# Kernel tuning notes

Measured on AMD Instinct MI355X. Metric: run time of the kernel, lower is better.

The kernel has to match this reference:

```python
import jax, jax.numpy as jnp
import numpy as np

N = 100000   # nodes
E = 1600000  # edges (before self-loops)
H1, C1 = 8, 16   # conv1: heads=8, out_channels=16
H2, C2 = 1, 1    # conv2: heads=1, out_channels=1
NEG_SLOPE = 0.2
EPS = 1e-16


def setup_inputs() -> dict:
    key = jax.random.key(0)
    ks = jax.random.split(key, 10)
    s = 0.3
    return {
        "x": jax.random.normal(ks[0], (N, 1), jnp.float32),
        "edge_index": jax.random.randint(ks[1], (2, E), 0, N, dtype=jnp.int64),
        "W1": jax.random.normal(ks[2], (1, H1 * C1), jnp.float32) * s,
        "att_src1": jax.random.normal(ks[3], (1, H1, C1), jnp.float32) * s,
        "att_dst1": jax.random.normal(ks[4], (1, H1, C1), jnp.float32) * s,
        "b1": jax.random.normal(ks[5], (H1 * C1,), jnp.float32) * s,
        "W2": jax.random.normal(ks[6], (H1 * C1, H2 * C2), jnp.float32) * s,
        "att_src2": jax.random.normal(ks[7], (1, H2, C2), jnp.float32) * s,
        "att_dst2": jax.random.normal(ks[8], (1, H2, C2), jnp.float32) * s,
        "b2": jax.random.normal(ks[9], (C2,), jnp.float32) * s,
    }


def gat_conv(x, src, dst, W, att_src, att_dst, bias, heads, ch, concat):
    # Linear projection, split into heads: [N, H, C]
    h = (x @ W).reshape(-1, heads, ch)
    # Per-node attention logits: [N, H]
    a_src = (h * att_src).sum(-1)
    a_dst = (h * att_dst).sum(-1)
    # Edge-wise score with LeakyReLU: [E, H]
    e = jax.nn.leaky_relu(a_src[src] + a_dst[dst], NEG_SLOPE)
    # Segment softmax over incoming edges of each dst node
    m = jax.ops.segment_max(e, dst, num_segments=N)
    ex = jnp.exp(e - m[dst])
    denom = jax.ops.segment_sum(ex, dst, num_segments=N)
    alpha = ex / (denom[dst] + EPS)                      # [E, H]
    # Weighted scatter-add aggregation: [N, H, C]
    out = jax.ops.segment_sum(h[src] * alpha[:, :, None], dst, num_segments=N)
    out = out.reshape(-1, heads * ch) if concat else out.mean(axis=1)
    return out + bias


def reference(x, edge_index, W1, att_src1, att_dst1, b1, W2, att_src2, att_dst2, b2):
    # PyG GATConv default add_self_loops=True
    loop = jnp.arange(N, dtype=edge_index.dtype)
    src = jnp.concatenate([edge_index[0], loop])
    dst = jnp.concatenate([edge_index[1], loop])
    # dropout p=0.6 is identity in eval mode
    h = gat_conv(x, src, dst, W1, att_src1, att_dst1, b1, H1, C1, concat=True)
    h = jax.nn.elu(h)
    out = gat_conv(h, src, dst, W2, att_src2, att_dst2, b2, H2, C2, concat=False)
    return out  # [N, 1]
```

## Files before the change

### kernel.cpp

```cpp
#include <hip/hip_runtime.h>

#define NEG_SLOPE 0.2f
#define EPSV 1e-16f
#define NHEADS 8
#define NCH 16
#define BKT_SHIFT 8
#define BKT_NODES 256
#define CAP 8192
#define BIN_EPB 4096
#define MAX_BKT 512

__global__ __launch_bounds__(512) void gat_setup_kernel(
        const float* __restrict__ W1, const float* __restrict__ as1,
        const float* __restrict__ ad1, float* __restrict__ S1,
        float* __restrict__ D1, int* __restrict__ bkt_cnt, int nbuckets) {
    int t = threadIdx.x;
    for (int i = t; i < nbuckets; i += 512) bkt_cnt[i] = 0;
    if (t < NHEADS) {
        float s = 0.f, d = 0.f;
        for (int c = 0; c < NCH; ++c) {
            float w = W1[t * NCH + c];
            s += w * as1[t * NCH + c];
            d += w * ad1[t * NCH + c];
        }
        S1[t] = s;
        D1[t] = d;
    }
}

__global__ __launch_bounds__(256) void gat_bin_kernel(
        const int* __restrict__ ei, int E, int nbuckets,
        int* __restrict__ bkt_cnt, unsigned int* __restrict__ binned) {
    __shared__ int hist[MAX_BKT];
    __shared__ int gbase[MAX_BKT];
    int t = threadIdx.x;
    for (int i = t; i < nbuckets; i += 256) hist[i] = 0;
    __syncthreads();
    int base = blockIdx.x * BIN_EPB;
    int lr[BIN_EPB / 256];
#pragma unroll
    for (int k = 0; k < BIN_EPB / 1024; ++k) {
        int idx = base + k * 1024 + t * 4;
        if (idx + 3 < E) {
            int4 d4 = *(const int4*)(ei + E + idx);
            lr[4 * k + 0] = atomicAdd(&hist[d4.x >> BKT_SHIFT], 1);
            lr[4 * k + 1] = atomicAdd(&hist[d4.y >> BKT_SHIFT], 1);
            lr[4 * k + 2] = atomicAdd(&hist[d4.z >> BKT_SHIFT], 1);
            lr[4 * k + 3] = atomicAdd(&hist[d4.w >> BKT_SHIFT], 1);
        } else {
            for (int u = 0; u < 4; ++u)
                if (idx + u < E)
                    lr[4 * k + u] = atomicAdd(&hist[ei[E + idx + u] >> BKT_SHIFT], 1);
        }
    }
    __syncthreads();
    for (int i = t; i < nbuckets; i += 256) {
        int c = hist[i];
        gbase[i] = c ? (i * CAP + atomicAdd(&bkt_cnt[i], c)) : 0;
    }
    __syncthreads();
#pragma unroll
    for (int k = 0; k < BIN_EPB / 1024; ++k) {
        int idx = base + k * 1024 + t * 4;
        if (idx + 3 < E) {
            int4 s4 = *(const int4*)(ei + idx);
            int4 d4 = *(const int4*)(ei + E + idx);
            binned[gbase[d4.x >> BKT_SHIFT] + lr[4 * k + 0]] =
                ((unsigned int)s4.x << BKT_SHIFT) | (unsigned int)(d4.x & (BKT_NODES - 1));
            binned[gbase[d4.y >> BKT_SHIFT] + lr[4 * k + 1]] =
                ((unsigned int)s4.y << BKT_SHIFT) | (unsigned int)(d4.y & (BKT_NODES - 1));
            binned[gbase[d4.z >> BKT_SHIFT] + lr[4 * k + 2]] =
                ((unsigned int)s4.z << BKT_SHIFT) | (unsigned int)(d4.z & (BKT_NODES - 1));
            binned[gbase[d4.w >> BKT_SHIFT] + lr[4 * k + 3]] =
                ((unsigned int)s4.w << BKT_SHIFT) | (unsigned int)(d4.w & (BKT_NODES - 1));
        } else {
            for (int u = 0; u < 4; ++u)
                if (idx + u < E) {
                    unsigned int s = (unsigned int)ei[idx + u];
                    int d = ei[E + idx + u];
                    binned[gbase[d >> BKT_SHIFT] + lr[4 * k + u]] =
                        (s << BKT_SHIFT) | (unsigned int)(d & (BKT_NODES - 1));
                }
        }
    }
}

__global__ __launch_bounds__(256) void gat_gather1_kernel(
        int N, const float* __restrict__ x,
        unsigned int* __restrict__ binned, const int* __restrict__ bkt_cnt,
        const float* __restrict__ S1g, const float* __restrict__ D1g,
        const float* __restrict__ W1, const float* __restrict__ b1,
        const float* __restrict__ W2, float* __restrict__ h2out,
        int* __restrict__ row_start, int* __restrict__ row_deg) {
    __shared__ unsigned int ed[CAP];
    __shared__ int cnt[BKT_NODES];
    __shared__ int off[BKT_NODES];
    __shared__ int cur[BKT_NODES];
    __shared__ float xloc[BKT_NODES];
    int b = blockIdx.x, t = threadIdx.x;
    int node = (b << BKT_SHIFT) + t;
    xloc[t] = (node < N) ? x[node] : 0.f;
    cnt[t] = 0;
    __syncthreads();
    int nE = bkt_cnt[b]; if (nE > CAP) nE = CAP;
    const unsigned int* bb = binned + (size_t)b * CAP;
    for (int j0 = 0; j0 < nE; j0 += 1024) {
        int idx = j0 + t * 4;
        if (idx + 3 < nE) {
            uint4 q = *(const uint4*)(bb + idx);
            atomicAdd(&cnt[q.x & (BKT_NODES - 1)], 1);
            atomicAdd(&cnt[q.y & (BKT_NODES - 1)], 1);
            atomicAdd(&cnt[q.z & (BKT_NODES - 1)], 1);
            atomicAdd(&cnt[q.w & (BKT_NODES - 1)], 1);
        } else {
            for (int u = 0; u < 4; ++u)
                if (idx + u < nE) atomicAdd(&cnt[bb[idx + u] & (BKT_NODES - 1)], 1);
        }
    }
    __syncthreads();
    int c = cnt[t];
    off[t] = c;
    __syncthreads();
    for (int o = 1; o < 256; o <<= 1) {
        int v = (t >= o) ? off[t - o] : 0;
        __syncthreads();
        off[t] += v;
        __syncthreads();
    }
    int o_excl = off[t] - c;
    off[t] = o_excl;
    cur[t] = o_excl;
    __syncthreads();
    for (int j0 = 0; j0 < nE; j0 += 1024) {
        int idx = j0 + t * 4;
        if (idx + 3 < nE) {
            uint4 q = *(const uint4*)(bb + idx);
            ed[atomicAdd(&cur[q.x & (BKT_NODES - 1)], 1)] = q.x >> BKT_SHIFT;
            ed[atomicAdd(&cur[q.y & (BKT_NODES - 1)], 1)] = q.y >> BKT_SHIFT;
            ed[atomicAdd(&cur[q.z & (BKT_NODES - 1)], 1)] = q.z >> BKT_SHIFT;
            ed[atomicAdd(&cur[q.w & (BKT_NODES - 1)], 1)] = q.w >> BKT_SHIFT;
        } else {
            for (int u = 0; u < 4; ++u)
                if (idx + u < nE) {
                    unsigned int v = bb[idx + u];
                    ed[atomicAdd(&cur[v & (BKT_NODES - 1)], 1)] = v >> BKT_SHIFT;
                }
        }
    }
    __syncthreads();
    for (int j0 = 0; j0 < nE; j0 += 1024) {
        int idx = j0 + t * 4;
        if (idx + 3 < nE) {
            *(uint4*)(binned + (size_t)b * CAP + idx) = *(const uint4*)(ed + idx);
        } else {
            for (int u = 0; u < 4; ++u)
                if (idx + u < nE) binned[(size_t)b * CAP + idx + u] = ed[idx + u];
        }
    }
    if (node < N) {
        row_start[node] = b * CAP + o_excl;
        row_deg[node] = c;
    }
    float S1[NHEADS], A[NHEADS], den[NHEADS], num[NHEADS];
    float xn = xloc[t];
#pragma unroll
    for (int h = 0; h < NHEADS; ++h) {
        S1[h] = S1g[h];
        A[h] = xn * D1g[h];
        float e = xn * S1[h] + A[h];
        e = e > 0.f ? e : NEG_SLOPE * e;
        float ex = __expf(e);
        den[h] = ex + EPSV;
        num[h] = ex * xn;
    }
    int j = 0;
    for (; j + 4 <= c; j += 4) {
        unsigned int e0 = ed[o_excl + j + 0], e1 = ed[o_excl + j + 1];
        unsigned int e2 = ed[o_excl + j + 2], e3 = ed[o_excl + j + 3];
        float x0 = x[e0], x1 = x[e1], x2 = x[e2], x3 = x[e3];
#pragma unroll
        for (int h = 0; h < NHEADS; ++h) {
            float ea = x0 * S1[h] + A[h]; ea = ea > 0.f ? ea : NEG_SLOPE * ea;
            float eb = x1 * S1[h] + A[h]; eb = eb > 0.f ? eb : NEG_SLOPE * eb;
            float ec = x2 * S1[h] + A[h]; ec = ec > 0.f ? ec : NEG_SLOPE * ec;
            float ee = x3 * S1[h] + A[h]; ee = ee > 0.f ? ee : NEG_SLOPE * ee;
            float fa = __expf(ea), fb = __expf(eb), fc = __expf(ec), fd = __expf(ee);
            den[h] += (fa + fb) + (fc + fd);
            num[h] += (fa * x0 + fb * x1) + (fc * x2 + fd * x3);
        }
    }
    for (; j < c; ++j) {
        unsigned int e0 = ed[o_excl + j];
        float x0 = x[e0];
#pragma unroll
        for (int h = 0; h < NHEADS; ++h) {
            float ea = x0 * S1[h] + A[h];
            ea = ea > 0.f ? ea : NEG_SLOPE * ea;
            float fa = __expf(ea);
            den[h] += fa;
            num[h] += fa * x0;
        }
    }
    if (node >= N) return;
    float acc = 0.f;
#pragma unroll
    for (int h = 0; h < NHEADS; ++h) {
        float z = num[h] / den[h];
#pragma unroll
        for (int cc = 0; cc < NCH; ++cc) {
            int k = h * NCH + cc;
            float vv = W1[k] * z + b1[k];
            vv = vv > 0.f ? vv : (__expf(vv) - 1.f);
            acc += vv * W2[k];
        }
    }
    h2out[node] = acc;
}

__global__ __launch_bounds__(256) void gat_gather2_kernel(
        int N, const float* __restrict__ h2,
        const unsigned int* __restrict__ binned,
        const int* __restrict__ row_start, const int* __restrict__ row_deg,
        const float* __restrict__ as2p, const float* __restrict__ ad2p,
        const float* __restrict__ b2, float* __restrict__ out) {
    int n = blockIdx.x * blockDim.x + threadIdx.x;
    if (n >= N) return;
    float a_s = as2p[0], a_d = ad2p[0];
    float hn = h2[n];
    float ad = hn * a_d;
    float e = hn * a_s + ad;
    e = e > 0.f ? e : NEG_SLOPE * e;
    float ex = __expf(e);
    float den = ex + EPSV;
    float num = ex * hn;
    int st = row_start[n], dg = row_deg[n];
    int j = 0;
    for (; j + 4 <= dg; j += 4) {
        unsigned int e0 = binned[st + j + 0], e1 = binned[st + j + 1];
        unsigned int e2 = binned[st + j + 2], e3 = binned[st + j + 3];
        float h0 = h2[e0], h1 = h2[e1], h3 = h2[e2], h4 = h2[e3];
        float ea = h0 * a_s + ad; ea = ea > 0.f ? ea : NEG_SLOPE * ea;
        float eb = h1 * a_s + ad; eb = eb > 0.f ? eb : NEG_SLOPE * eb;
        float ec = h3 * a_s + ad; ec = ec > 0.f ? ec : NEG_SLOPE * ec;
        float ee = h4 * a_s + ad; ee = ee > 0.f ? ee : NEG_SLOPE * ee;
        float fa = __expf(ea), fb = __expf(eb), fc = __expf(ec), fd = __expf(ee);
        den += (fa + fb) + (fc + fd);
        num += (fa * h0 + fb * h1) + (fc * h3 + fd * h4);
    }
    for (; j < dg; ++j) {
        unsigned int e0 = binned[st + j];
        float h0 = h2[e0];
        float ea = h0 * a_s + ad;
        ea = ea > 0.f ? ea : NEG_SLOPE * ea;
        float fa = __expf(ea);
        den += fa;
        num += fa * h0;
    }
    out[n] = num / den + b2[0];
}

extern "C" void kernel_launch(void* const* d_in, const int* in_sizes, int n_in,
                              void* d_out, int out_size, void* d_ws, size_t ws_size,
                              hipStream_t stream) {
    const float* x   = (const float*)d_in[0];
    const int*   ei  = (const int*)d_in[1];
    const float* W1  = (const float*)d_in[2];
    const float* as1 = (const float*)d_in[3];
    const float* ad1 = (const float*)d_in[4];
    const float* b1  = (const float*)d_in[5];
    const float* W2  = (const float*)d_in[6];
    const float* as2 = (const float*)d_in[7];
    const float* ad2 = (const float*)d_in[8];
    const float* b2  = (const float*)d_in[9];
    float* out = (float*)d_out;

    int N = in_sizes[0];
    int E = in_sizes[1] / 2;

    int nbuckets = (N + BKT_NODES - 1) >> BKT_SHIFT;
    int nbin     = (E + BIN_EPB - 1) / BIN_EPB;
    int nb       = (N + 255) / 256;

    float* S1        = (float*)d_ws;
    float* D1        = S1 + 8;
    float* h2        = D1 + 8;
    int*   row_start = (int*)(h2 + N);
    int*   row_deg   = row_start + N;
    int*   bkt_cnt   = row_deg + N;
    unsigned int* binned = (unsigned int*)(bkt_cnt + nbuckets);

    gat_setup_kernel<<<1, 512, 0, stream>>>(W1, as1, ad1, S1, D1,
                                            bkt_cnt, nbuckets);
    gat_bin_kernel<<<nbin, 256, 0, stream>>>(ei, E, nbuckets, bkt_cnt, binned);
    gat_gather1_kernel<<<nbuckets, 256, 0, stream>>>(N, x, binned, bkt_cnt,
                                                     S1, D1, W1, b1, W2, h2,
                                                     row_start, row_deg);
    gat_gather2_kernel<<<nb, 256, 0, stream>>>(N, h2, binned, row_start, row_deg,
                                               as2, ad2, b2, out);
}
```

Baseline: 132.5 us.

## Split each node's edges across two lanes and shrink buckets to 128 nodes

Buckets shrink to 128 nodes with capacity 4096, so gather1 runs more blocks. Each destination node is now handled by two lanes that interleave its edges and combine partial sums with a shuffle, and the per-head MLP epilogue is split between the two lanes. The bin kernel uses 512 threads with 8192 edges per block and keeps destination indices in registers instead of reloading them. Gather1 keeps its bucket's edges in registers rather than reading them twice from global memory. The fixed 16-entry register array assumes at most 4096 edges per bucket, so larger buckets would be truncated as before.

```diff
diff --git a/kernel.cpp b/kernel.cpp
--- a/kernel.cpp
+++ b/kernel.cpp
@@ -4,11 +4,12 @@
 #define EPSV 1e-16f
 #define NHEADS 8
 #define NCH 16
-#define BKT_SHIFT 8
-#define BKT_NODES 256
-#define CAP 8192
-#define BIN_EPB 4096
-#define MAX_BKT 512
+#define BKT_SHIFT 7
+#define BKT_NODES 128
+#define CAP 4096
+#define BIN_TPB 512
+#define BIN_EPB 8192
+#define MAX_BKT 1024
 
 __global__ __launch_bounds__(512) void gat_setup_kernel(
         const float* __restrict__ W1, const float* __restrict__ as1,
@@ -28,56 +29,59 @@
     }
 }
 
-__global__ __launch_bounds__(256) void gat_bin_kernel(
+__global__ __launch_bounds__(BIN_TPB) void gat_bin_kernel(
         const int* __restrict__ ei, int E, int nbuckets,
         int* __restrict__ bkt_cnt, unsigned int* __restrict__ binned) {
     __shared__ int hist[MAX_BKT];
     __shared__ int gbase[MAX_BKT];
     int t = threadIdx.x;
-    for (int i = t; i < nbuckets; i += 256) hist[i] = 0;
+    for (int i = t; i < nbuckets; i += BIN_TPB) hist[i] = 0;
     __syncthreads();
     int base = blockIdx.x * BIN_EPB;
-    int lr[BIN_EPB / 256];
-#pragma unroll
-    for (int k = 0; k < BIN_EPB / 1024; ++k) {
-        int idx = base + k * 1024 + t * 4;
+    int dv[16];
+    int lr[16];
+#pragma unroll
+    for (int k = 0; k < 4; ++k) {
+        int idx = base + k * (BIN_TPB * 4) + t * 4;
         if (idx + 3 < E) {
             int4 d4 = *(const int4*)(ei + E + idx);
-            lr[4 * k + 0] = atomicAdd(&hist[d4.x >> BKT_SHIFT], 1);
-            lr[4 * k + 1] = atomicAdd(&hist[d4.y >> BKT_SHIFT], 1);
-            lr[4 * k + 2] = atomicAdd(&hist[d4.z >> BKT_SHIFT], 1);
-            lr[4 * k + 3] = atomicAdd(&hist[d4.w >> BKT_SHIFT], 1);
+            dv[4 * k + 0] = d4.x; dv[4 * k + 1] = d4.y;
+            dv[4 * k + 2] = d4.z; dv[4 * k + 3] = d4.w;
         } else {
+#pragma unroll
             for (int u = 0; u < 4; ++u)
-                if (idx + u < E)
-                    lr[4 * k + u] = atomicAdd(&hist[ei[E + idx + u] >> BKT_SHIFT], 1);
-        }
-    }
-    __syncthreads();
-    for (int i = t; i < nbuckets; i += 256) {
+                dv[4 * k + u] = (idx + u < E) ? ei[E + idx + u] : -1;
+        }
+#pragma unroll
+        for (int u = 0; u < 4; ++u)
+            lr[4 * k + u] = (dv[4 * k + u] >= 0)
+                ? atomicAdd(&hist[dv[4 * k + u] >> BKT_SHIFT], 1) : 0;
+    }
+    __syncthreads();
+    for (int i = t; i < nbuckets; i += BIN_TPB) {
         int c = hist[i];
         gbase[i] = c ? (i * CAP + atomicAdd(&bkt_cnt[i], c)) : 0;
     }
     __syncthreads();
 #pragma unroll
-    for (int k = 0; k < BIN_EPB / 1024; ++k) {
-        int idx = base + k * 1024 + t * 4;
+    for (int k = 0; k < 4; ++k) {
+        int idx = base + k * (BIN_TPB * 4) + t * 4;
         if (idx + 3 < E) {
             int4 s4 = *(const int4*)(ei + idx);
-            int4 d4 = *(const int4*)(ei + E + idx);
-            binned[gbase[d4.x >> BKT_SHIFT] + lr[4 * k + 0]] =
-                ((unsigned int)s4.x << BKT_SHIFT) | (unsigned int)(d4.x & (BKT_NODES - 1));
-            binned[gbase[d4.y >> BKT_SHIFT] + lr[4 * k + 1]] =
-                ((unsigned int)s4.y << BKT_SHIFT) | (unsigned int)(d4.y & (BKT_NODES - 1));
-            binned[gbase[d4.z >> BKT_SHIFT] + lr[4 * k + 2]] =
-                ((unsigned int)s4.z << BKT_SHIFT) | (unsigned int)(d4.z & (BKT_NODES - 1));
-            binned[gbase[d4.w >> BKT_SHIFT] + lr[4 * k + 3]] =
-                ((unsigned int)s4.w << BKT_SHIFT) | (unsigned int)(d4.w & (BKT_NODES - 1));
+            binned[gbase[dv[4 * k + 0] >> BKT_SHIFT] + lr[4 * k + 0]] =
+                ((unsigned int)s4.x << BKT_SHIFT) | (unsigned int)(dv[4 * k + 0] & (BKT_NODES - 1));
+            binned[gbase[dv[4 * k + 1] >> BKT_SHIFT] + lr[4 * k + 1]] =
+                ((unsigned int)s4.y << BKT_SHIFT) | (unsigned int)(dv[4 * k + 1] & (BKT_NODES - 1));
+            binned[gbase[dv[4 * k + 2] >> BKT_SHIFT] + lr[4 * k + 2]] =
+                ((unsigned int)s4.z << BKT_SHIFT) | (unsigned int)(dv[4 * k + 2] & (BKT_NODES - 1));
+            binned[gbase[dv[4 * k + 3] >> BKT_SHIFT] + lr[4 * k + 3]] =
+                ((unsigned int)s4.w << BKT_SHIFT) | (unsigned int)(dv[4 * k + 3] & (BKT_NODES - 1));
         } else {
+#pragma unroll
             for (int u = 0; u < 4; ++u)
                 if (idx + u < E) {
                     unsigned int s = (unsigned int)ei[idx + u];
-                    int d = ei[E + idx + u];
+                    int d = dv[4 * k + u];
                     binned[gbase[d >> BKT_SHIFT] + lr[4 * k + u]] =
                         (s << BKT_SHIFT) | (unsigned int)(d & (BKT_NODES - 1));
                 }
@@ -98,55 +102,58 @@
     __shared__ int cur[BKT_NODES];
     __shared__ float xloc[BKT_NODES];
     int b = blockIdx.x, t = threadIdx.x;
-    int node = (b << BKT_SHIFT) + t;
-    xloc[t] = (node < N) ? x[node] : 0.f;
-    cnt[t] = 0;
+    int r = t & 1, nl = t >> 1;
+    int node = (b << BKT_SHIFT) + nl;
+    if (t < BKT_NODES) {
+        int nn = (b << BKT_SHIFT) + t;
+        xloc[t] = (nn < N) ? x[nn] : 0.f;
+        cnt[t] = 0;
+    }
     __syncthreads();
     int nE = bkt_cnt[b]; if (nE > CAP) nE = CAP;
     const unsigned int* bb = binned + (size_t)b * CAP;
-    for (int j0 = 0; j0 < nE; j0 += 1024) {
-        int idx = j0 + t * 4;
+    unsigned int qa[16];
+#pragma unroll
+    for (int k = 0; k < 4; ++k) {
+        int idx = k * 1024 + t * 4;
         if (idx + 3 < nE) {
-            uint4 q = *(const uint4*)(bb + idx);
-            atomicAdd(&cnt[q.x & (BKT_NODES - 1)], 1);
-            atomicAdd(&cnt[q.y & (BKT_NODES - 1)], 1);
-            atomicAdd(&cnt[q.z & (BKT_NODES - 1)], 1);
-            atomicAdd(&cnt[q.w & (BKT_NODES - 1)], 1);
+            uint4 v4 = *(const uint4*)(bb + idx);
+            qa[4 * k + 0] = v4.x; qa[4 * k + 1] = v4.y;
+            qa[4 * k + 2] = v4.z; qa[4 * k + 3] = v4.w;
         } else {
+#pragma unroll
             for (int u = 0; u < 4; ++u)
-                if (idx + u < nE) atomicAdd(&cnt[bb[idx + u] & (BKT_NODES - 1)], 1);
-        }
-    }
-    __syncthreads();
-    int c = cnt[t];
-    off[t] = c;
-    __syncthreads();
-    for (int o = 1; o < 256; o <<= 1) {
-        int v = (t >= o) ? off[t - o] : 0;
+                qa[4 * k + u] = (idx + u < nE) ? bb[idx + u] : 0xFFFFFFFFu;
+        }
+#pragma unroll
+        for (int u = 0; u < 4; ++u)
+            if (qa[4 * k + u] != 0xFFFFFFFFu)
+                atomicAdd(&cnt[qa[4 * k + u] & (BKT_NODES - 1)], 1);
+    }
+    __syncthreads();
+    int c0 = (t < BKT_NODES) ? cnt[t] : 0;
+    if (t < BKT_NODES) off[t] = c0;
+    __syncthreads();
+    for (int o = 1; o < BKT_NODES; o <<= 1) {
+        int v = (t >= o && t < BKT_NODES) ? off[t - o] : 0;
         __syncthreads();
-        off[t] += v;
+        if (t < BKT_NODES) off[t] += v;
         __syncthreads();
     }
-    int o_excl = off[t] - c;
-    off[t] = o_excl;
-    cur[t] = o_excl;
-    __syncthreads();
-    for (int j0 = 0; j0 < nE; j0 += 1024) {
-        int idx = j0 + t * 4;
-        if (idx + 3 < nE) {
-            uint4 q = *(const uint4*)(bb + idx);
-            ed[atomicAdd(&cur[q.x & (BKT_NODES - 1)], 1)] = q.x >> BKT_SHIFT;
-            ed[atomicAdd(&cur[q.y & (BKT_NODES - 1)], 1)] = q.y >> BKT_SHIFT;
-            ed[atomicAdd(&cur[q.z & (BKT_NODES - 1)], 1)] = q.z >> BKT_SHIFT;
-            ed[atomicAdd(&cur[q.w & (BKT_NODES - 1)], 1)] = q.w >> BKT_SHIFT;
-        } else {
-            for (int u = 0; u < 4; ++u)
-                if (idx + u < nE) {
-                    unsigned int v = bb[idx + u];
-                    ed[atomicAdd(&cur[v & (BKT_NODES - 1)], 1)] = v >> BKT_SHIFT;
-                }
-        }
-    }
+    if (t < BKT_NODES) {
+        int oe = off[t] - c0;
+        off[t] = oe;
+        cur[t] = oe;
+    }
+    __syncthreads();
+#pragma unroll
+    for (int k = 0; k < 4; ++k)
+#pragma unroll
+        for (int u = 0; u < 4; ++u) {
+            unsigned int v = qa[4 * k + u];
+            if (v != 0xFFFFFFFFu)
+                ed[atomicAdd(&cur[v & (BKT_NODES - 1)], 1)] = v >> BKT_SHIFT;
+        }
     __syncthreads();
     for (int j0 = 0; j0 < nE; j0 += 1024) {
         int idx = j0 + t * 4;
@@ -157,12 +164,14 @@
                 if (idx + u < nE) binned[(size_t)b * CAP + idx + u] = ed[idx + u];
         }
     }
-    if (node < N) {
-        row_start[node] = b * CAP + o_excl;
+    int myoff = off[nl];
+    int c = cnt[nl];
+    if (r == 0 && node < N) {
+        row_start[node] = b * CAP + myoff;
         row_deg[node] = c;
     }
     float S1[NHEADS], A[NHEADS], den[NHEADS], num[NHEADS];
-    float xn = xloc[t];
+    float xn = (node < N) ? xloc[nl] : 0.f;
 #pragma unroll
     for (int h = 0; h < NHEADS; ++h) {
         S1[h] = S1g[h];
@@ -170,13 +179,13 @@
         float e = xn * S1[h] + A[h];
         e = e > 0.f ? e : NEG_SLOPE * e;
         float ex = __expf(e);
-        den[h] = ex + EPSV;
-        num[h] = ex * xn;
-    }
-    int j = 0;
-    for (; j + 4 <= c; j += 4) {
-        unsigned int e0 = ed[o_excl + j + 0], e1 = ed[o_excl + j + 1];
-        unsigned int e2 = ed[o_excl + j + 2], e3 = ed[o_excl + j + 3];
+        den[h] = r ? 0.f : ex + EPSV;
+        num[h] = r ? 0.f : ex * xn;
+    }
+    int j = r;
+    for (; j + 6 < c; j += 8) {
+        unsigned int e0 = ed[myoff + j + 0], e1 = ed[myoff + j + 2];
+        unsigned int e2 = ed[myoff + j + 4], e3 = ed[myoff + j + 6];
         float x0 = x[e0], x1 = x[e1], x2 = x[e2], x3 = x[e3];
 #pragma unroll
         for (int h = 0; h < NHEADS; ++h) {
@@ -189,8 +198,8 @@
             num[h] += (fa * x0 + fb * x1) + (fc * x2 + fd * x3);
         }
     }
-    for (; j < c; ++j) {
-        unsigned int e0 = ed[o_excl + j];
+    for (; j < c; j += 2) {
+        unsigned int e0 = ed[myoff + j];
         float x0 = x[e0];
 #pragma unroll
         for (int h = 0; h < NHEADS; ++h) {
@@ -201,20 +210,28 @@
             num[h] += fa * x0;
         }
     }
-    if (node >= N) return;
+#pragma unroll
+    for (int h = 0; h < NHEADS; ++h) {
+        den[h] += __shfl_xor(den[h], 1);
+        num[h] += __shfl_xor(num[h], 1);
+    }
     float acc = 0.f;
-#pragma unroll
-    for (int h = 0; h < NHEADS; ++h) {
-        float z = num[h] / den[h];
+    int hbase = r * 4;
+#pragma unroll
+    for (int hp = 0; hp < 4; ++hp) {
+        float nh = r ? num[hp + 4] : num[hp];
+        float dh = r ? den[hp + 4] : den[hp];
+        float z = nh / dh;
+        int kb = (hbase + hp) * NCH;
 #pragma unroll
         for (int cc = 0; cc < NCH; ++cc) {
-            int k = h * NCH + cc;
-            float vv = W1[k] * z + b1[k];
+            float vv = W1[kb + cc] * z + b1[kb + cc];
             vv = vv > 0.f ? vv : (__expf(vv) - 1.f);
-            acc += vv * W2[k];
-        }
-    }
-    h2out[node] = acc;
+            acc += vv * W2[kb + cc];
+        }
+    }
+    acc += __shfl_xor(acc, 1);
+    if (r == 0 && node < N) h2out[node] = acc;
 }
 
 __global__ __launch_bounds__(256) void gat_gather2_kernel(
@@ -223,7 +240,9 @@
         const int* __restrict__ row_start, const int* __restrict__ row_deg,
         const float* __restrict__ as2p, const float* __restrict__ ad2p,
         const float* __restrict__ b2, float* __restrict__ out) {
-    int n = blockIdx.x * blockDim.x + threadIdx.x;
+    int t = threadIdx.x;
+    int r = t & 1;
+    int n = blockIdx.x * 128 + (t >> 1);
     if (n >= N) return;
     float a_s = as2p[0], a_d = ad2p[0];
     float hn = h2[n];
@@ -231,13 +250,13 @@
     float e = hn * a_s + ad;
     e = e > 0.f ? e : NEG_SLOPE * e;
     float ex = __expf(e);
-    float den = ex + EPSV;
-    float num = ex * hn;
+    float den = r ? 0.f : ex + EPSV;
+    float num = r ? 0.f : ex * hn;
     int st = row_start[n], dg = row_deg[n];
-    int j = 0;
-    for (; j + 4 <= dg; j += 4) {
-        unsigned int e0 = binned[st + j + 0], e1 = binned[st + j + 1];
-        unsigned int e2 = binned[st + j + 2], e3 = binned[st + j + 3];
+    int j = r;
+    for (; j + 6 < dg; j += 8) {
+        unsigned int e0 = binned[st + j + 0], e1 = binned[st + j + 2];
+        unsigned int e2 = binned[st + j + 4], e3 = binned[st + j + 6];
         float h0 = h2[e0], h1 = h2[e1], h3 = h2[e2], h4 = h2[e3];
         float ea = h0 * a_s + ad; ea = ea > 0.f ? ea : NEG_SLOPE * ea;
         float eb = h1 * a_s + ad; eb = eb > 0.f ? eb : NEG_SLOPE * eb;
@@ -247,7 +266,7 @@
         den += (fa + fb) + (fc + fd);
         num += (fa * h0 + fb * h1) + (fc * h3 + fd * h4);
     }
-    for (; j < dg; ++j) {
+    for (; j < dg; j += 2) {
         unsigned int e0 = binned[st + j];
         float h0 = h2[e0];
         float ea = h0 * a_s + ad;
@@ -256,7 +275,9 @@
         den += fa;
         num += fa * h0;
     }
-    out[n] = num / den + b2[0];
+    den += __shfl_xor(den, 1);
+    num += __shfl_xor(num, 1);
+    if (r == 0) out[n] = num / den + b2[0];
 }
 
 extern "C" void kernel_launch(void* const* d_in, const int* in_sizes, int n_in,
@@ -279,7 +300,7 @@
 
     int nbuckets = (N + BKT_NODES - 1) >> BKT_SHIFT;
     int nbin     = (E + BIN_EPB - 1) / BIN_EPB;
-    int nb       = (N + 255) / 256;
+    int nb       = (N + 127) / 128;
 
     float* S1        = (float*)d_ws;
     float* D1        = S1 + 8;
@@ -291,7 +312,7 @@
 
     gat_setup_kernel<<<1, 512, 0, stream>>>(W1, as1, ad1, S1, D1,
                                             bkt_cnt, nbuckets);
-    gat_bin_kernel<<<nbin, 256, 0, stream>>>(ei, E, nbuckets, bkt_cnt, binned);
+    gat_bin_kernel<<<nbin, BIN_TPB, 0, stream>>>(ei, E, nbuckets, bkt_cnt, binned);
     gat_gather1_kernel<<<nbuckets, 256, 0, stream>>>(N, x, binned, bkt_cnt,
                                                      S1, D1, W1, b1, W2, h2,
                                                      row_start, row_deg);
```

Result: slower. 135.6 us (+2.3%).

## Fuse all GAT stages into one cooperative kernel with grid syncs

Applied to the files above, without the earlier changes.

Merges setup, edge binning, layer-1 gather and layer-2 gather into a single cooperative-launch kernel, one block per 256-node bucket, separated by grid-wide syncs. The per-node sorted edge lists stay in shared memory between layers, so the row_start/row_deg arrays and the rewrite of sorted edges to global memory are dropped. This removes three kernel launches and one round trip through global memory, but binning now runs on only ~391 blocks looping over chunks, and the large shared-memory union may limit residency. It falls back to the old kernels if the cooperative launch fails.

```diff
diff --git a/kernel.cpp b/kernel.cpp
--- a/kernel.cpp
+++ b/kernel.cpp
@@ -1,4 +1,7 @@
 #include <hip/hip_runtime.h>
+#include <hip/hip_cooperative_groups.h>
+
+namespace cg = cooperative_groups;
 
 #define NEG_SLOPE 0.2f
 #define EPSV 1e-16f
@@ -9,6 +12,232 @@
 #define CAP 8192
 #define BIN_EPB 4096
 #define MAX_BKT 512
+
+struct BinSM  { int hist[MAX_BKT]; int gbase[MAX_BKT]; };
+struct GathSM { unsigned int ed[CAP]; int cnt[BKT_NODES];
+                int off[BKT_NODES]; int cur[BKT_NODES]; };
+union  SMU    { BinSM bin; GathSM g; };
+
+__global__ __launch_bounds__(256) void gat_fused_kernel(
+        int N, int E, const float* __restrict__ x, const int* __restrict__ ei,
+        const float* __restrict__ W1, const float* __restrict__ as1,
+        const float* __restrict__ ad1, const float* __restrict__ b1,
+        const float* __restrict__ W2, const float* __restrict__ as2,
+        const float* __restrict__ ad2, const float* __restrict__ b2,
+        float* __restrict__ h2, int* __restrict__ bkt_cnt,
+        unsigned int* __restrict__ binned, float* __restrict__ out) {
+    cg::grid_group grid = cg::this_grid();
+    __shared__ SMU sm;
+    __shared__ float S1s[NHEADS], D1s[NHEADS], xloc[BKT_NODES];
+    int b = blockIdx.x, t = threadIdx.x;
+    int nbuckets = gridDim.x;
+
+    if (t == 0) bkt_cnt[b] = 0;
+    grid.sync();
+
+    int nchunks = (E + BIN_EPB - 1) / BIN_EPB;
+    for (int ch = b; ch < nchunks; ch += gridDim.x) {
+        for (int i = t; i < nbuckets; i += 256) sm.bin.hist[i] = 0;
+        __syncthreads();
+        int base = ch * BIN_EPB;
+        int lr[16];
+#pragma unroll
+        for (int k = 0; k < 4; ++k) {
+            int idx = base + k * 1024 + t * 4;
+            if (idx + 3 < E) {
+                int4 d4 = *(const int4*)(ei + E + idx);
+                lr[4*k+0] = atomicAdd(&sm.bin.hist[d4.x >> BKT_SHIFT], 1);
+                lr[4*k+1] = atomicAdd(&sm.bin.hist[d4.y >> BKT_SHIFT], 1);
+                lr[4*k+2] = atomicAdd(&sm.bin.hist[d4.z >> BKT_SHIFT], 1);
+                lr[4*k+3] = atomicAdd(&sm.bin.hist[d4.w >> BKT_SHIFT], 1);
+            } else {
+                for (int u = 0; u < 4; ++u)
+                    if (idx + u < E)
+                        lr[4*k+u] = atomicAdd(&sm.bin.hist[ei[E + idx + u] >> BKT_SHIFT], 1);
+            }
+        }
+        __syncthreads();
+        for (int i = t; i < nbuckets; i += 256) {
+            int c = sm.bin.hist[i];
+            sm.bin.gbase[i] = c ? (i * CAP + atomicAdd(&bkt_cnt[i], c)) : 0;
+        }
+        __syncthreads();
+#pragma unroll
+        for (int k = 0; k < 4; ++k) {
+            int idx = base + k * 1024 + t * 4;
+            if (idx + 3 < E) {
+                int4 s4 = *(const int4*)(ei + idx);
+                int4 d4 = *(const int4*)(ei + E + idx);
+                binned[sm.bin.gbase[d4.x >> BKT_SHIFT] + lr[4*k+0]] =
+                    ((unsigned)s4.x << BKT_SHIFT) | (unsigned)(d4.x & (BKT_NODES-1));
+                binned[sm.bin.gbase[d4.y >> BKT_SHIFT] + lr[4*k+1]] =
+                    ((unsigned)s4.y << BKT_SHIFT) | (unsigned)(d4.y & (BKT_NODES-1));
+                binned[sm.bin.gbase[d4.z >> BKT_SHIFT] + lr[4*k+2]] =
+                    ((unsigned)s4.z << BKT_SHIFT) | (unsigned)(d4.z & (BKT_NODES-1));
+                binned[sm.bin.gbase[d4.w >> BKT_SHIFT] + lr[4*k+3]] =
+                    ((unsigned)s4.w << BKT_SHIFT) | (unsigned)(d4.w & (BKT_NODES-1));
+            } else {
+                for (int u = 0; u < 4; ++u)
+                    if (idx + u < E) {
+                        unsigned s = (unsigned)ei[idx + u];
+                        int d = ei[E + idx + u];
+                        binned[sm.bin.gbase[d >> BKT_SHIFT] + lr[4*k+u]] =
+                            (s << BKT_SHIFT) | (unsigned)(d & (BKT_NODES-1));
+                    }
+            }
+        }
+        __syncthreads();
+    }
+    grid.sync();
+
+    if (t < NHEADS) {
+        float s = 0.f, d = 0.f;
+        for (int c = 0; c < NCH; ++c) {
+            float w = W1[t * NCH + c];
+            s += w * as1[t * NCH + c];
+            d += w * ad1[t * NCH + c];
+        }
+        S1s[t] = s; D1s[t] = d;
+    }
+    int node = (b << BKT_SHIFT) + t;
+    xloc[t] = (node < N) ? x[node] : 0.f;
+    sm.g.cnt[t] = 0;
+    __syncthreads();
+    int nE = bkt_cnt[b]; if (nE > CAP) nE = CAP;
+    const unsigned int* bb = binned + (size_t)b * CAP;
+    for (int j0 = 0; j0 < nE; j0 += 1024) {
+        int idx = j0 + t * 4;
+        if (idx + 3 < nE) {
+            uint4 q = *(const uint4*)(bb + idx);
+            atomicAdd(&sm.g.cnt[q.x & (BKT_NODES-1)], 1);
+            atomicAdd(&sm.g.cnt[q.y & (BKT_NODES-1)], 1);
+            atomicAdd(&sm.g.cnt[q.z & (BKT_NODES-1)], 1);
+            atomicAdd(&sm.g.cnt[q.w & (BKT_NODES-1)], 1);
+        } else {
+            for (int u = 0; u < 4; ++u)
+                if (idx + u < nE) atomicAdd(&sm.g.cnt[bb[idx + u] & (BKT_NODES-1)], 1);
+        }
+    }
+    __syncthreads();
+    int c = sm.g.cnt[t];
+    sm.g.off[t] = c;
+    __syncthreads();
+    for (int o = 1; o < 256; o <<= 1) {
+        int v = (t >= o) ? sm.g.off[t - o] : 0;
+        __syncthreads();
+        sm.g.off[t] += v;
+        __syncthreads();
+    }
+    int o_excl = sm.g.off[t] - c;
+    sm.g.off[t] = o_excl;
+    sm.g.cur[t] = o_excl;
+    __syncthreads();
+    for (int j0 = 0; j0 < nE; j0 += 1024) {
+        int idx = j0 + t * 4;
+        if (idx + 3 < nE) {
+            uint4 q = *(const uint4*)(bb + idx);
+            sm.g.ed[atomicAdd(&sm.g.cur[q.x & (BKT_NODES-1)], 1)] = q.x >> BKT_SHIFT;
+            sm.g.ed[atomicAdd(&sm.g.cur[q.y & (BKT_NODES-1)], 1)] = q.y >> BKT_SHIFT;
+            sm.g.ed[atomicAdd(&sm.g.cur[q.z & (BKT_NODES-1)], 1)] = q.z >> BKT_SHIFT;
+            sm.g.ed[atomicAdd(&sm.g.cur[q.w & (BKT_NODES-1)], 1)] = q.w >> BKT_SHIFT;
+        } else {
+            for (int u = 0; u < 4; ++u)
+                if (idx + u < nE) {
+                    unsigned v = bb[idx + u];
+                    sm.g.ed[atomicAdd(&sm.g.cur[v & (BKT_NODES-1)], 1)] = v >> BKT_SHIFT;
+                }
+        }
+    }
+    __syncthreads();
+    float S1[NHEADS], A[NHEADS], den[NHEADS], num[NHEADS];
+    float xn = xloc[t];
+#pragma unroll
+    for (int h = 0; h < NHEADS; ++h) {
+        S1[h] = S1s[h];
+        A[h] = xn * D1s[h];
+        float e = xn * S1[h] + A[h];
+        e = e > 0.f ? e : NEG_SLOPE * e;
+        float ex = __expf(e);
+        den[h] = ex + EPSV;
+        num[h] = ex * xn;
+    }
+    int j = 0;
+    for (; j + 4 <= c; j += 4) {
+        unsigned e0 = sm.g.ed[o_excl + j + 0], e1 = sm.g.ed[o_excl + j + 1];
+        unsigned e2 = sm.g.ed[o_excl + j + 2], e3 = sm.g.ed[o_excl + j + 3];
+        float x0 = x[e0], x1 = x[e1], x2 = x[e2], x3 = x[e3];
+#pragma unroll
+        for (int h = 0; h < NHEADS; ++h) {
+            float ea = x0 * S1[h] + A[h]; ea = ea > 0.f ? ea : NEG_SLOPE * ea;
+            float eb = x1 * S1[h] + A[h]; eb = eb > 0.f ? eb : NEG_SLOPE * eb;
+            float ec = x2 * S1[h] + A[h]; ec = ec > 0.f ? ec : NEG_SLOPE * ec;
+            float ee = x3 * S1[h] + A[h]; ee = ee > 0.f ? ee : NEG_SLOPE * ee;
+            float fa = __expf(ea), fb = __expf(eb), fc = __expf(ec), fd = __expf(ee);
+            den[h] += (fa + fb) + (fc + fd);
+            num[h] += (fa * x0 + fb * x1) + (fc * x2 + fd * x3);
+        }
+    }
+    for (; j < c; ++j) {
+        unsigned e0 = sm.g.ed[o_excl + j];
+        float x0 = x[e0];
+#pragma unroll
+        for (int h = 0; h < NHEADS; ++h) {
+            float ea = x0 * S1[h] + A[h];
+            ea = ea > 0.f ? ea : NEG_SLOPE * ea;
+            float fa = __expf(ea);
+            den[h] += fa;
+            num[h] += fa * x0;
+        }
+    }
+    float acc = 0.f;
+#pragma unroll
+    for (int h = 0; h < NHEADS; ++h) {
+        float z = num[h] / den[h];
+#pragma unroll
+        for (int cc = 0; cc < NCH; ++cc) {
+            int k = h * NCH + cc;
+            float vv = W1[k] * z + b1[k];
+            vv = vv > 0.f ? vv : (__expf(vv) - 1.f);
+            acc += vv * W2[k];
+        }
+    }
+    if (node < N) h2[node] = acc;
+    grid.sync();
+
+    if (node < N) {
+        float a_s = as2[0], a_d = ad2[0];
+        float hn = acc;
+        float ad = hn * a_d;
+        float e = hn * a_s + ad;
+        e = e > 0.f ? e : NEG_SLOPE * e;
+        float ex = __expf(e);
+        float dn2 = ex + EPSV;
+        float nm2 = ex * hn;
+        int jj = 0;
+        for (; jj + 4 <= c; jj += 4) {
+            unsigned e0 = sm.g.ed[o_excl + jj + 0], e1 = sm.g.ed[o_excl + jj + 1];
+            unsigned e2 = sm.g.ed[o_excl + jj + 2], e3 = sm.g.ed[o_excl + jj + 3];
+            float h0 = h2[e0], h1 = h2[e1], h3 = h2[e2], h4 = h2[e3];
+            float ea = h0 * a_s + ad; ea = ea > 0.f ? ea : NEG_SLOPE * ea;
+            float eb = h1 * a_s + ad; eb = eb > 0.f ? eb : NEG_SLOPE * eb;
+            float ec = h3 * a_s + ad; ec = ec > 0.f ? ec : NEG_SLOPE * ec;
+            float ee = h4 * a_s + ad; ee = ee > 0.f ? ee : NEG_SLOPE * ee;
+            float fa = __expf(ea), fb = __expf(eb), fc = __expf(ec), fd = __expf(ee);
+            dn2 += (fa + fb) + (fc + fd);
+            nm2 += (fa * h0 + fb * h1) + (fc * h3 + fd * h4);
+        }
+        for (; jj < c; ++jj) {
+            unsigned e0 = sm.g.ed[o_excl + jj];
+            float h0 = h2[e0];
+            float ea = h0 * a_s + ad;
+            ea = ea > 0.f ? ea : NEG_SLOPE * ea;
+            float fa = __expf(ea);
+            dn2 += fa;
+            nm2 += fa * h0;
+        }
+        out[node] = nm2 / dn2 + b2[0];
+    }
+}
 
 __global__ __launch_bounds__(512) void gat_setup_kernel(
         const float* __restrict__ W1, const float* __restrict__ as1,
@@ -37,20 +266,20 @@
     for (int i = t; i < nbuckets; i += 256) hist[i] = 0;
     __syncthreads();
     int base = blockIdx.x * BIN_EPB;
-    int lr[BIN_EPB / 256];
-#pragma unroll
-    for (int k = 0; k < BIN_EPB / 1024; ++k) {
+    int lr[16];
+#pragma unroll
+    for (int k = 0; k < 4; ++k) {
         int idx = base + k * 1024 + t * 4;
         if (idx + 3 < E) {
             int4 d4 = *(const int4*)(ei + E + idx);
-            lr[4 * k + 0] = atomicAdd(&hist[d4.x >> BKT_SHIFT], 1);
-            lr[4 * k + 1] = atomicAdd(&hist[d4.y >> BKT_SHIFT], 1);
-            lr[4 * k + 2] = atomicAdd(&hist[d4.z >> BKT_SHIFT], 1);
-            lr[4 * k + 3] = atomicAdd(&hist[d4.w >> BKT_SHIFT], 1);
+            lr[4*k+0] = atomicAdd(&hist[d4.x >> BKT_SHIFT], 1);
+            lr[4*k+1] = atomicAdd(&hist[d4.y >> BKT_SHIFT], 1);
+            lr[4*k+2] = atomicAdd(&hist[d4.z >> BKT_SHIFT], 1);
+            lr[4*k+3] = atomicAdd(&hist[d4.w >> BKT_SHIFT], 1);
         } else {
             for (int u = 0; u < 4; ++u)
                 if (idx + u < E)
-                    lr[4 * k + u] = atomicAdd(&hist[ei[E + idx + u] >> BKT_SHIFT], 1);
+                    lr[4*k+u] = atomicAdd(&hist[ei[E + idx + u] >> BKT_SHIFT], 1);
         }
     }
     __syncthreads();
@@ -60,26 +289,26 @@
     }
     __syncthreads();
 #pragma unroll
-    for (int k = 0; k < BIN_EPB / 1024; ++k) {
+    for (int k = 0; k < 4; ++k) {
         int idx = base + k * 1024 + t * 4;
         if (idx + 3 < E) {
             int4 s4 = *(const int4*)(ei + idx);
             int4 d4 = *(const int4*)(ei + E + idx);
-            binned[gbase[d4.x >> BKT_SHIFT] + lr[4 * k + 0]] =
-                ((unsigned int)s4.x << BKT_SHIFT) | (unsigned int)(d4.x & (BKT_NODES - 1));
-            binned[gbase[d4.y >> BKT_SHIFT] + lr[4 * k + 1]] =
-                ((unsigned int)s4.y << BKT_SHIFT) | (unsigned int)(d4.y & (BKT_NODES - 1));
-            binned[gbase[d4.z >> BKT_SHIFT] + lr[4 * k + 2]] =
-                ((unsigned int)s4.z << BKT_SHIFT) | (unsigned int)(d4.z & (BKT_NODES - 1));
-            binned[gbase[d4.w >> BKT_SHIFT] + lr[4 * k + 3]] =
-                ((unsigned int)s4.w << BKT_SHIFT) | (unsigned int)(d4.w & (BKT_NODES - 1));
+            binned[gbase[d4.x >> BKT_SHIFT] + lr[4*k+0]] =
+                ((unsigned)s4.x << BKT_SHIFT) | (unsigned)(d4.x & (BKT_NODES-1));
+            binned[gbase[d4.y >> BKT_SHIFT] + lr[4*k+1]] =
+                ((unsigned)s4.y << BKT_SHIFT) | (unsigned)(d4.y & (BKT_NODES-1));
+            binned[gbase[d4.z >> BKT_SHIFT] + lr[4*k+2]] =
+                ((unsigned)s4.z << BKT_SHIFT) | (unsigned)(d4.z & (BKT_NODES-1));
+            binned[gbase[d4.w >> BKT_SHIFT] + lr[4*k+3]] =
+                ((unsigned)s4.w << BKT_SHIFT) | (unsigned)(d4.w & (BKT_NODES-1));
         } else {
             for (int u = 0; u < 4; ++u)
                 if (idx + u < E) {
-                    unsigned int s = (unsigned int)ei[idx + u];
+                    unsigned s = (unsigned)ei[idx + u];
                     int d = ei[E + idx + u];
-                    binned[gbase[d >> BKT_SHIFT] + lr[4 * k + u]] =
-                        (s << BKT_SHIFT) | (unsigned int)(d & (BKT_NODES - 1));
+                    binned[gbase[d >> BKT_SHIFT] + lr[4*k+u]] =
+                        (s << BKT_SHIFT) | (unsigned)(d & (BKT_NODES-1));
                 }
         }
     }
@@ -108,13 +337,13 @@
         int idx = j0 + t * 4;
         if (idx + 3 < nE) {
             uint4 q = *(const uint4*)(bb + idx);
-            atomicAdd(&cnt[q.x & (BKT_NODES - 1)], 1);
-            atomicAdd(&cnt[q.y & (BKT_NODES - 1)], 1);
-            atomicAdd(&cnt[q.z & (BKT_NODES - 1)], 1);
-            atomicAdd(&cnt[q.w & (BKT_NODES - 1)], 1);
-        } else {
-            for (int u = 0; u < 4; ++u)
-                if (idx + u < nE) atomicAdd(&cnt[bb[idx + u] & (BKT_NODES - 1)], 1);
+            atomicAdd(&cnt[q.x & (BKT_NODES-1)], 1);
+            atomicAdd(&cnt[q.y & (BKT_NODES-1)], 1);
+            atomicAdd(&cnt[q.z & (BKT_NODES-1)], 1);
+            atomicAdd(&cnt[q.w & (BKT_NODES-1)], 1);
+        } else {
+            for (int u = 0; u < 4; ++u)
+                if (idx + u < nE) atomicAdd(&cnt[bb[idx + u] & (BKT_NODES-1)], 1);
         }
     }
     __syncthreads();
@@ -135,15 +364,15 @@
         int idx = j0 + t * 4;
         if (idx + 3 < nE) {
             uint4 q = *(const uint4*)(bb + idx);
-            ed[atomicAdd(&cur[q.x & (BKT_NODES - 1)], 1)] = q.x >> BKT_SHIFT;
-            ed[atomicAdd(&cur[q.y & (BKT_NODES - 1)], 1)] = q.y >> BKT_SHIFT;
-            ed[atomicAdd(&cur[q.z & (BKT_NODES - 1)], 1)] = q.z >> BKT_SHIFT;
-            ed[atomicAdd(&cur[q.w & (BKT_NODES - 1)], 1)] = q.w >> BKT_SHIFT;
+            ed[atomicAdd(&cur[q.x & (BKT_NODES-1)], 1)] = q.x >> BKT_SHIFT;
+            ed[atomicAdd(&cur[q.y & (BKT_NODES-1)], 1)] = q.y >> BKT_SHIFT;
+            ed[atomicAdd(&cur[q.z & (BKT_NODES-1)], 1)] = q.z >> BKT_SHIFT;
+            ed[atomicAdd(&cur[q.w & (BKT_NODES-1)], 1)] = q.w >> BKT_SHIFT;
         } else {
             for (int u = 0; u < 4; ++u)
                 if (idx + u < nE) {
-                    unsigned int v = bb[idx + u];
-                    ed[atomicAdd(&cur[v & (BKT_NODES - 1)], 1)] = v >> BKT_SHIFT;
+                    unsigned v = bb[idx + u];
+                    ed[atomicAdd(&cur[v & (BKT_NODES-1)], 1)] = v >> BKT_SHIFT;
                 }
         }
     }
@@ -175,8 +404,8 @@
     }
     int j = 0;
     for (; j + 4 <= c; j += 4) {
-        unsigned int e0 = ed[o_excl + j + 0], e1 = ed[o_excl + j + 1];
-        unsigned int e2 = ed[o_excl + j + 2], e3 = ed[o_excl + j + 3];
+        unsigned e0 = ed[o_excl + j + 0], e1 = ed[o_excl + j + 1];
+        unsigned e2 = ed[o_excl + j + 2], e3 = ed[o_excl + j + 3];
         float x0 = x[e0], x1 = x[e1], x2 = x[e2], x3 = x[e3];
 #pragma unroll
         for (int h = 0; h < NHEADS; ++h) {
@@ -190,7 +419,7 @@
         }
     }
     for (; j < c; ++j) {
-        unsigned int e0 = ed[o_excl + j];
+        unsigned e0 = ed[o_excl + j];
         float x0 = x[e0];
 #pragma unroll
         for (int h = 0; h < NHEADS; ++h) {
@@ -236,8 +465,8 @@
     int st = row_start[n], dg = row_deg[n];
     int j = 0;
     for (; j + 4 <= dg; j += 4) {
-        unsigned int e0 = binned[st + j + 0], e1 = binned[st + j + 1];
-        unsigned int e2 = binned[st + j + 2], e3 = binned[st + j + 3];
+        unsigned e0 = binned[st + j + 0], e1 = binned[st + j + 1];
+        unsigned e2 = binned[st + j + 2], e3 = binned[st + j + 3];
         float h0 = h2[e0], h1 = h2[e1], h3 = h2[e2], h4 = h2[e3];
         float ea = h0 * a_s + ad; ea = ea > 0.f ? ea : NEG_SLOPE * ea;
         float eb = h1 * a_s + ad; eb = eb > 0.f ? eb : NEG_SLOPE * eb;
@@ -248,7 +477,7 @@
         num += (fa * h0 + fb * h1) + (fc * h3 + fd * h4);
     }
     for (; j < dg; ++j) {
-        unsigned int e0 = binned[st + j];
+        unsigned e0 = binned[st + j];
         float h0 = h2[e0];
         float ea = h0 * a_s + ad;
         ea = ea > 0.f ? ea : NEG_SLOPE * ea;
@@ -278,8 +507,6 @@
     int E = in_sizes[1] / 2;
 
     int nbuckets = (N + BKT_NODES - 1) >> BKT_SHIFT;
-    int nbin     = (E + BIN_EPB - 1) / BIN_EPB;
-    int nb       = (N + 255) / 256;
 
     float* S1        = (float*)d_ws;
     float* D1        = S1 + 8;
@@ -289,6 +516,16 @@
     int*   bkt_cnt   = row_deg + N;
     unsigned int* binned = (unsigned int*)(bkt_cnt + nbuckets);
 
+    void* args[] = { (void*)&N, (void*)&E, (void*)&x, (void*)&ei,
+                     (void*)&W1, (void*)&as1, (void*)&ad1, (void*)&b1,
+                     (void*)&W2, (void*)&as2, (void*)&ad2, (void*)&b2,
+                     (void*)&h2, (void*)&bkt_cnt, (void*)&binned, (void*)&out };
+    hipError_t err = hipLaunchCooperativeKernel(
+        gat_fused_kernel, dim3(nbuckets), dim3(256), args, 0u, stream);
+    if (err == hipSuccess) return;
+
+    int nbin = (E + BIN_EPB - 1) / BIN_EPB;
+    int nb   = (N + 255) / 256;
     gat_setup_kernel<<<1, 512, 0, stream>>>(W1, as1, ad1, S1, D1,
                                             bkt_cnt, nbuckets);
     gat_bin_kernel<<<nbin, 256, 0, stream>>>(ei, E, nbuckets, bkt_cnt, binned);
```

Measured after the change: 275.9 us. 2.08x slower.
